# Kernel tuning notes

Hardware: AMD Instinct MI355X
Metric: run time of the kernel (lower is better)

The kernel has to match this reference:

```python
import jax, jax.numpy as jnp
import numpy as np
import math

B, T, D = 2, 2048, 1024
H, DH = 16, 64  # n_heads, d_head
ROPE_THETA = 10000.0


def _rope_cos_sin(seq_len, d_head, dtype):
    # inv_freq over even indices, freqs[i,j] = t_i * inv_freq_j, shape [T, d_head//2]
    inv_freq = 1.0 / (ROPE_THETA ** (jnp.arange(0, d_head, 2, dtype=jnp.float32) / d_head))
    freqs = jnp.arange(seq_len, dtype=jnp.float32)[:, None] * inv_freq[None, :]
    # emb = cat(freqs, freqs); we only ever index cos[..., :d_head//2], so keep the half
    cos = jnp.cos(freqs).astype(dtype)[None, :, None, :]  # [1,T,1,DH/2]
    sin = jnp.sin(freqs).astype(dtype)[None, :, None, :]
    return cos, sin


def _apply_rotation(x, cos, sin):
    # x: [B,T,H,DH]; rotate-half style as in the torch module
    x1, x2 = x[..., : x.shape[-1] // 2], x[..., x.shape[-1] // 2 :]
    return jnp.concatenate([x1 * cos - x2 * sin, x1 * sin + x2 * cos], axis=-1)


def setup_inputs() -> dict:
    key = jax.random.key(0)
    k1, k2, k3 = jax.random.split(key, 3)
    x = jax.random.normal(k1, (B, T, D), dtype=jnp.float32)
    # torch Linear weights stored transposed here as [in, out]; init_std=0.02
    Wqkv = jax.random.normal(k2, (D, 3 * D), dtype=jnp.float32) * 0.02
    Wout = jax.random.normal(k3, (D, D), dtype=jnp.float32) * 0.02
    return {"x": x, "Wqkv": Wqkv, "Wout": Wout}


def reference(x, Wqkv, Wout):
    b, t, d = x.shape
    qkv = x @ Wqkv  # [B,T,3D]
    q, k, v = jnp.split(qkv, 3, axis=-1)
    q = q.reshape(b, t, H, DH)
    k = k.reshape(b, t, H, DH)
    v = v.reshape(b, t, H, DH)

    cos, sin = _rope_cos_sin(t, DH, x.dtype)
    q = _apply_rotation(q, cos, sin)
    k = _apply_rotation(k, cos, sin)

    scale = 1.0 / math.sqrt(DH)
    # scores: [B,H,Tq,Tk]
    scores = jnp.einsum("bqhd,bkhd->bhqk", q, k) * scale
    causal = jnp.triu(jnp.ones((t, t), dtype=bool), k=1)
    scores = jnp.where(causal[None, None, :, :], -jnp.inf, scores)
    attn = jax.nn.softmax(scores, axis=-1)
    # dropout in eval mode -> identity
    out = jnp.einsum("bhqk,bkhd->bqhd", attn, v).reshape(b, t, d)
    return out @ Wout
```

## Files before the change

### kernel.cpp

```cpp
#include <hip/hip_runtime.h>
#include <hip/hip_bf16.h>
#include <stdint.h>
#include <math.h>

#define T_SEQ 2048
#define NHEAD 16
#define NBH   32
#define BTROW 4096

typedef __bf16 bf16_t;
typedef __bf16 bf16x4_t __attribute__((ext_vector_type(4)));
typedef __bf16 bf16x8_t __attribute__((ext_vector_type(8)));
typedef float  f32x4_t  __attribute__((ext_vector_type(4)));

#define QSCALE 0.18033688011112042f

__device__ __forceinline__ f32x4_t mfma16(bf16x8_t a, bf16x8_t b, f32x4_t c) {
  return __builtin_amdgcn_mfma_f32_16x16x32_bf16(a, b, c, 0, 0, 0);
}

__device__ __forceinline__ float fast_exp2(float x) {
#if __has_builtin(__builtin_amdgcn_exp2f)
  return __builtin_amdgcn_exp2f(x);
#else
  return exp2f(x);
#endif
}

__device__ __forceinline__ void gl_lds16(const bf16_t* g, bf16_t* l) {
  __builtin_amdgcn_global_load_lds(
      (const __attribute__((address_space(1))) void*)g,
      (__attribute__((address_space(3))) void*)l, 16, 0, 0);
}

__global__ __launch_bounds__(256) void k_cast_bf16(const float* __restrict__ in,
                                                   bf16_t* __restrict__ out, int n) {
  int tid = blockIdx.x * blockDim.x + threadIdx.x;
  int stride = gridDim.x * blockDim.x;
  for (int i = tid * 4; i < n; i += stride * 4) {
    float4 a = *(const float4*)(in + i);
    bf16x4_t r = { (bf16_t)a.x, (bf16_t)a.y, (bf16_t)a.z, (bf16_t)a.w };
    *(bf16x4_t*)(out + i) = r;
  }
}

__global__ __launch_bounds__(256) void k_trans_cast(const float* __restrict__ W,
                                                    bf16_t* __restrict__ WT,
                                                    int K, int N) {
  __shared__ float tile[32][33];
  int n0 = blockIdx.x * 32, k0 = blockIdx.y * 32;
  int tx = threadIdx.x & 31, ty = threadIdx.x >> 5;
#pragma unroll
  for (int j = 0; j < 4; j++)
    tile[ty + j * 8][tx] = W[(size_t)(k0 + ty + j * 8) * N + n0 + tx];
  __syncthreads();
#pragma unroll
  for (int j = 0; j < 4; j++)
    WT[(size_t)(n0 + ty + j * 8) * K + k0 + tx] = (bf16_t)tile[tx][ty + j * 8];
}

__global__ __launch_bounds__(256) void k_rope_table(float* __restrict__ cs,
                                                    float* __restrict__ sn) {
  int i = blockIdx.x * blockDim.x + threadIdx.x;
  if (i >= T_SEQ * 32) return;
  int t = i >> 5, j = i & 31;
  float inv = powf(10000.0f, -(float)(2 * j) / 64.0f);
  float f = (float)t * inv;
  cs[i] = cosf(f);
  sn[i] = sinf(f);
}

__global__ __launch_bounds__(256) void k_gemm_qkv(const bf16_t* __restrict__ A,
                                                  const bf16_t* __restrict__ Bt,
                                                  const float* __restrict__ cs,
                                                  const float* __restrict__ sn,
                                                  bf16_t* __restrict__ Qr,
                                                  bf16_t* __restrict__ Kr,
                                                  bf16_t* __restrict__ Vt) {
  const int K = 1024;
  __shared__ __align__(16) unsigned char smem[33792];
  bf16_t* vtile = (bf16_t*)smem;

  int m0 = blockIdx.y * 128, n0 = blockIdx.x * 128;
  int tid = threadIdx.x;
  int lane = tid & 63, w = tid >> 6;
  int wr = w >> 1, wc = w & 1;
  int l15 = lane & 15, l4 = lane >> 4;

  f32x4_t acc[4][4];
#pragma unroll
  for (int m = 0; m < 4; m++)
#pragma unroll
    for (int n = 0; n < 4; n++) acc[m][n] = (f32x4_t){0.f, 0.f, 0.f, 0.f};

  auto stageg = [&](int bf, int k0) {
    bf16_t* As = (bf16_t*)(smem + bf * 16384);
    bf16_t* Bs = (bf16_t*)(smem + 8192 + bf * 16384);
#pragma unroll
    for (int j = 0; j < 2; j++) {
      int c = j * 256 + tid;
      int row = c >> 2, kb = c & 3;
      gl_lds16(A + (size_t)(m0 + row) * K + k0 + kb * 8, As + (size_t)(j * 256 + w * 64) * 8);
      gl_lds16(Bt + (size_t)(n0 + row) * K + k0 + kb * 8, Bs + (size_t)(j * 256 + w * 64) * 8);
    }
  };

  stageg(0, 0);
  for (int kt = 0; kt < 32; kt++) {
    int cb = kt & 1;
    bf16_t* As = (bf16_t*)(smem + cb * 16384);
    bf16_t* Bs = (bf16_t*)(smem + 8192 + cb * 16384);
    asm volatile("s_waitcnt vmcnt(0)" ::: "memory");
    __builtin_amdgcn_s_barrier();
    if (kt + 1 < 32) stageg(cb ^ 1, (kt + 1) * 32);
    bf16x8_t af[4], bfr[4];
#pragma unroll
    for (int m = 0; m < 4; m++)
      af[m] = *(const bf16x8_t*)(As + (size_t)(wr * 64 + m * 16 + l15) * 32 + l4 * 8);
#pragma unroll
    for (int n = 0; n < 4; n++)
      bfr[n] = *(const bf16x8_t*)(Bs + (size_t)(wc * 64 + n * 16 + l15) * 32 + l4 * 8);
#pragma unroll
    for (int m = 0; m < 4; m++)
#pragma unroll
      for (int n = 0; n < 4; n++) acc[m][n] = mfma16(af[m], bfr[n], acc[m][n]);
  }
  __syncthreads();

  int region = n0 >> 10;
  if (region < 2) {
    bf16_t* dst = region ? Kr : Qr;
    float qs = region ? 1.0f : QSCALE;
    int h = ((n0 & 1023) + wc * 64) >> 6;
#pragma unroll
    for (int m = 0; m < 4; m++)
#pragma unroll
      for (int r = 0; r < 4; r++) {
        int row = m0 + wr * 64 + m * 16 + l4 * 4 + r;
        int b = row >> 11, t = row & 2047;
        size_t obase = ((size_t)(b * NHEAD + h) * T_SEQ + t) * 64;
#pragma unroll
        for (int n = 0; n < 2; n++) {
          int j = n * 16 + l15;
          float c = cs[t * 32 + j], s = sn[t * 32 + j];
          float x1 = acc[m][n][r], x2 = acc[m][n + 2][r];
          dst[obase + j]      = (bf16_t)((x1 * c - x2 * s) * qs);
          dst[obase + 32 + j] = (bf16_t)((x1 * s + x2 * c) * qs);
        }
      }
  } else {
#pragma unroll
    for (int m = 0; m < 4; m++)
#pragma unroll
      for (int n = 0; n < 4; n++)
#pragma unroll
        for (int r = 0; r < 4; r++)
          vtile[(size_t)(wc * 64 + n * 16 + l15) * 132 + wr * 64 + m * 16 + l4 * 4 + r] =
              (bf16_t)acc[m][n][r];
    __syncthreads();
    int colbase = n0 - 2048;
    int b = m0 >> 11, t0l = m0 & 2047;
#pragma unroll
    for (int p = 0; p < 64; p++) {
      int idx = p * 256 + tid;
      int dl = idx >> 7, tl = idx & 127;
      int col = colbase + dl, h = col >> 6, d = col & 63;
      Vt[((size_t)(b * NHEAD + h) * 64 + d) * T_SEQ + t0l + tl] = vtile[(size_t)dl * 132 + tl];
    }
  }
}

__global__ __launch_bounds__(256) void k_gemm2(const bf16_t* __restrict__ A,
                                               const bf16_t* __restrict__ Bt,
                                               float* __restrict__ C) {
  const int N = 1024, K = 1024;
  __shared__ __align__(16) bf16_t As[2][64 * 32];
  __shared__ __align__(16) bf16_t Bs[2][128 * 32];
  int m0 = blockIdx.y * 64, n0 = blockIdx.x * 128;
  int tid = threadIdx.x;
  int lane = tid & 63, w = tid >> 6;
  int l15 = lane & 15, l4 = lane >> 4;

  f32x4_t acc[4][2];
#pragma unroll
  for (int m = 0; m < 4; m++)
#pragma unroll
    for (int n = 0; n < 2; n++) acc[m][n] = (f32x4_t){0.f, 0.f, 0.f, 0.f};

  auto stageg = [&](int bf, int k0) {
    {
      int row = tid >> 2, kb = tid & 3;
      gl_lds16(A + (size_t)(m0 + row) * K + k0 + kb * 8, &As[bf][0] + (size_t)(w * 64) * 8);
    }
#pragma unroll
    for (int j = 0; j < 2; j++) {
      int c = j * 256 + tid;
      int row = c >> 2, kb = c & 3;
      gl_lds16(Bt + (size_t)(n0 + row) * K + k0 + kb * 8, &Bs[bf][0] + (size_t)(j * 256 + w * 64) * 8);
    }
  };

  stageg(0, 0);
  for (int kt = 0; kt < 32; kt++) {
    int cb = kt & 1;
    asm volatile("s_waitcnt vmcnt(0)" ::: "memory");
    __builtin_amdgcn_s_barrier();
    if (kt + 1 < 32) stageg(cb ^ 1, (kt + 1) * 32);
    bf16x8_t af[4], bfr[2];
#pragma unroll
    for (int m = 0; m < 4; m++)
      af[m] = *(const bf16x8_t*)(&As[cb][0] + (size_t)(m * 16 + l15) * 32 + l4 * 8);
#pragma unroll
    for (int n = 0; n < 2; n++)
      bfr[n] = *(const bf16x8_t*)(&Bs[cb][0] + (size_t)(w * 32 + n * 16 + l15) * 32 + l4 * 8);
#pragma unroll
    for (int m = 0; m < 4; m++)
#pragma unroll
      for (int n = 0; n < 2; n++) acc[m][n] = mfma16(af[m], bfr[n], acc[m][n]);
  }
#pragma unroll
  for (int m = 0; m < 4; m++)
#pragma unroll
    for (int n = 0; n < 2; n++)
#pragma unroll
      for (int r = 0; r < 4; r++) {
        int row = m0 + m * 16 + l4 * 4 + r;
        int col = n0 + w * 32 + n * 16 + l15;
        C[(size_t)row * N + col] = acc[m][n][r];
      }
}

__global__ __launch_bounds__(512, 4) void k_attn(const bf16_t* __restrict__ Qr,
                                                 const bf16_t* __restrict__ Kr,
                                                 const bf16_t* __restrict__ Vt,
                                                 bf16_t* __restrict__ Ob) {
  __shared__ __align__(16) bf16_t Ks[2][2][64 * 64];
  __shared__ __align__(16) bf16_t Vs[2][2][64 * 64];
  __shared__ __align__(16) bf16_t Ps[8][16 * 64];
  int flat = blockIdx.x;
  int swz = (flat & 7) * 64 + (flat >> 3);
  int pair = swz & 15, bh = swz >> 4;
  int b = bh >> 4, h = bh & 15;
  int tid = threadIdx.x, lane = tid & 63, w = tid >> 6;
  int grp = w >> 2, wl = w & 3;
  int l15 = lane & 15, l4 = lane >> 4;

  const bf16_t* Kbh = Kr + (size_t)bh * T_SEQ * 64;
  const bf16_t* Vbh = Vt + (size_t)bh * 64 * T_SEQ;

  int srow = tid >> 3;
  int sk8 = (tid & 7) ^ (srow & 7);

  auto stage = [&](int buf, int i) {
#pragma unroll
    for (int tp = 0; tp < 2; tp++) {
      int kb = (2 * i + tp) * 64;
      gl_lds16(Kbh + (size_t)(kb + srow) * 64 + sk8 * 8, &Ks[buf][tp][0] + (size_t)w * 512);
      gl_lds16(Vbh + (size_t)srow * T_SEQ + kb + sk8 * 8, &Vs[buf][tp][0] + (size_t)w * 512);
    }
  };

  char* myPs = (char*)&Ps[w][0];

  bf16x8_t ones;
#pragma unroll
  for (int i = 0; i < 8; i++) ones[i] = (bf16_t)1.0f;

  for (int pass = 0; pass < 2; pass++) {
    int qb = pass ? (31 - pair) : pair;
    int q0 = qb * 64;
    int niter = (qb + 2) >> 1;

    bf16x8_t qf[2];
    size_t qbase = ((size_t)bh * T_SEQ + q0 + wl * 16 + l15) * 64;
    qf[0] = *(const bf16x8_t*)(Qr + qbase + l4 * 8);
    qf[1] = *(const bf16x8_t*)(Qr + qbase + 32 + l4 * 8);

    f32x4_t o[4];
#pragma unroll
    for (int n = 0; n < 4; n++) o[n] = (f32x4_t){0.f, 0.f, 0.f, 0.f};
    f32x4_t ls = (f32x4_t){0.f, 0.f, 0.f, 0.f};
    float m_s = -1e30f;

    stage(0, 0);

    for (int i = 0; i < niter; i++) {
      int cur = i & 1;
      asm volatile("s_waitcnt vmcnt(0)" ::: "memory");
      __builtin_amdgcn_s_barrier();
      if (i + 1 < niter) stage(cur ^ 1, i + 1);

      int t = 2 * i + grp;
      if (t <= qb) {
        const bf16_t* Kt = &Ks[cur][grp][0];
        const bf16_t* Vtl = &Vs[cur][grp][0];

        f32x4_t s[4];
        __builtin_amdgcn_s_setprio(1);
#pragma unroll
        for (int n = 0; n < 4; n++) {
          int rowK = n * 16 + l15;
          const bf16_t* kp = Kt + (size_t)rowK * 64;
          int sw = rowK & 7;
          bf16x8_t kf0 = *(const bf16x8_t*)(kp + (l4 ^ sw) * 8);
          bf16x8_t kf1 = *(const bf16x8_t*)(kp + ((l4 ^ 4) ^ sw) * 8);
          s[n] = (f32x4_t){0.f, 0.f, 0.f, 0.f};
          s[n] = mfma16(kf0, qf[0], s[n]);
          s[n] = mfma16(kf1, qf[1], s[n]);
        }
        __builtin_amdgcn_s_setprio(0);

        if (t == qb) {
#pragma unroll
          for (int n = 0; n < 4; n++)
#pragma unroll
            for (int r = 0; r < 4; r++)
              if (n * 16 + l4 * 4 + r > wl * 16 + l15) s[n][r] = -1e30f;
        }

        float t0 = fmaxf(fmaxf(s[0][0], s[0][1]), fmaxf(s[0][2], s[0][3]));
        float t1 = fmaxf(fmaxf(s[1][0], s[1][1]), fmaxf(s[1][2], s[1][3]));
        float t2 = fmaxf(fmaxf(s[2][0], s[2][1]), fmaxf(s[2][2], s[2][3]));
        float t3 = fmaxf(fmaxf(s[3][0], s[3][1]), fmaxf(s[3][2], s[3][3]));
        float mx = fmaxf(fmaxf(t0, t1), fmaxf(t2, t3));
        mx = fmaxf(mx, __shfl_xor(mx, 16, 64));
        mx = fmaxf(mx, __shfl_xor(mx, 32, 64));

        if (__any(mx - m_s > 8.0f)) {
          float mnew = fmaxf(m_s, mx);
          float alpha = fast_exp2(m_s - mnew);
          m_s = mnew;
          float ar[4];
#pragma unroll
          for (int r = 0; r < 4; r++) ar[r] = __shfl(alpha, l4 * 4 + r, 64);
#pragma unroll
          for (int n = 0; n < 4; n++)
#pragma unroll
            for (int r = 0; r < 4; r++) o[n][r] *= ar[r];
#pragma unroll
          for (int r = 0; r < 4; r++) ls[r] *= ar[r];
        }

#pragma unroll
        for (int n = 0; n < 4; n++) {
#pragma unroll
          for (int r = 0; r < 4; r++) s[n][r] = fast_exp2(s[n][r] - m_s);
          bf16x4_t pk = { (bf16_t)s[n][0], (bf16_t)s[n][1], (bf16_t)s[n][2], (bf16_t)s[n][3] };
          *(bf16x4_t*)(myPs + l15 * 128 +
                       ((((n << 1) | (l4 >> 1)) ^ (l15 & 7)) << 4) + ((l4 & 1) << 3)) = pk;
        }

        __builtin_amdgcn_s_setprio(1);
#pragma unroll
        for (int ks = 0; ks < 2; ks++) {
          bf16x8_t pa = *(const bf16x8_t*)(myPs + l15 * 128 +
                                           ((((ks << 2) | l4) ^ (l15 & 7)) << 4));
          ls = mfma16(pa, ones, ls);
#pragma unroll
          for (int n = 0; n < 4; n++) {
            int rowV = n * 16 + l15;
            bf16x8_t vf = *(const bf16x8_t*)(Vtl + (size_t)rowV * 64 +
                                             (((ks * 4 + l4) ^ (rowV & 7)) * 8));
            o[n] = mfma16(pa, vf, o[n]);
          }
        }
        __builtin_amdgcn_s_setprio(0);
      }
    }

    __syncthreads();
    float* mg = (float*)&Ks[0][0][0];
    int base = (wl * 64 + lane) * 25;
    if (grp == 1) {
#pragma unroll
      for (int n = 0; n < 4; n++)
#pragma unroll
        for (int r = 0; r < 4; r++) mg[base + n * 4 + r] = o[n][r];
#pragma unroll
      for (int r = 0; r < 4; r++) mg[base + 16 + r] = ls[r];
#pragma unroll
      for (int r = 0; r < 4; r++) mg[base + 20 + r] = __shfl(m_s, l4 * 4 + r, 64);
    }
    __syncthreads();
    if (grp == 0) {
#pragma unroll
      for (int r = 0; r < 4; r++) {
        float mA = __shfl(m_s, l4 * 4 + r, 64);
        float mB = mg[base + 20 + r];
        float mF = fmaxf(mA, mB);
        float fA = fast_exp2(mA - mF), fB = fast_exp2(mB - mF);
        float lF = ls[r] * fA + mg[base + 16 + r] * fB;
        float ir = 1.0f / lF;
        int q = q0 + wl * 16 + l4 * 4 + r;
        size_t off = ((size_t)(b * T_SEQ + q)) * 1024 + h * 64;
#pragma unroll
        for (int n = 0; n < 4; n++) {
          float val = o[n][r] * fA + mg[base + n * 4 + r] * fB;
          Ob[off + n * 16 + l15] = (bf16_t)(val * ir);
        }
      }
    }
    __syncthreads();
  }
}

extern "C" void kernel_launch(void* const* d_in, const int* in_sizes, int n_in,
                              void* d_out, int out_size, void* d_ws, size_t ws_size,
                              hipStream_t stream) {
  const float* x    = (const float*)d_in[0];
  const float* Wqkv = (const float*)d_in[1];
  const float* Wout = (const float*)d_in[2];
  float* out = (float*)d_out;
  char* ws = (char*)d_ws;

  bf16_t* wqkvT = (bf16_t*)(ws + 0);
  bf16_t* woutT = (bf16_t*)(ws + 6291456);
  bf16_t* xb    = (bf16_t*)(ws + 8388608);
  bf16_t* Qr    = (bf16_t*)(ws + 41943040);
  bf16_t* Kr    = (bf16_t*)(ws + 50331648);
  bf16_t* Vt    = (bf16_t*)(ws + 58720256);
  float*  cs    = (float*)(ws + 67108864);
  float*  sn    = (float*)(ws + 67371008);
  bf16_t* Ob    = xb;

  k_cast_bf16<<<2048, 256, 0, stream>>>(x, xb, 4096 * 1024);
  k_trans_cast<<<dim3(3072 / 32, 1024 / 32), 256, 0, stream>>>(Wqkv, wqkvT, 1024, 3072);
  k_trans_cast<<<dim3(1024 / 32, 1024 / 32), 256, 0, stream>>>(Wout, woutT, 1024, 1024);
  k_rope_table<<<(T_SEQ * 32) / 256, 256, 0, stream>>>(cs, sn);

  k_gemm_qkv<<<dim3(3072 / 128, 4096 / 128), 256, 0, stream>>>(xb, wqkvT, cs, sn, Qr, Kr, Vt);
  k_attn<<<512, 512, 0, stream>>>(Qr, Kr, Vt, Ob);
  k_gemm2<<<dim3(1024 / 128, 4096 / 64), 256, 0, stream>>>(Ob, woutT, out);
}
```

Before: 119.1 us.

## Triple-buffer GEMM k-loops and prefetch V fragments early in attention

Both GEMM kernels move from double to triple buffering, prefetching two k-tiles ahead and waiting on a partial vmcnt instead of draining all loads. This is meant to hide global-to-LDS latency, at the cost of more shared memory per block and possibly lower occupancy. In attention, V fragments are loaded into registers right after the QK MFMAs so the LDS reads overlap the softmax. The row-max shuffles now run only when a rescale is triggered, which adds register pressure from the eight held V fragments.

```diff
diff --git a/kernel.cpp b/kernel.cpp
--- a/kernel.cpp
+++ b/kernel.cpp
@@ -77,8 +77,8 @@
                                                   bf16_t* __restrict__ Qr,
                                                   bf16_t* __restrict__ Kr,
                                                   bf16_t* __restrict__ Vt) {
-  const int K = 1024;
-  __shared__ __align__(16) unsigned char smem[33792];
+  const int K = 1024, NT = 32;
+  __shared__ __align__(16) unsigned char smem[49152];
   bf16_t* vtile = (bf16_t*)smem;
 
   int m0 = blockIdx.y * 128, n0 = blockIdx.x * 128;
@@ -106,13 +106,16 @@
   };
 
   stageg(0, 0);
-  for (int kt = 0; kt < 32; kt++) {
-    int cb = kt & 1;
+  stageg(1, 32);
+  for (int kt = 0; kt < NT; kt++) {
+    int cb = kt % 3;
     bf16_t* As = (bf16_t*)(smem + cb * 16384);
     bf16_t* Bs = (bf16_t*)(smem + 8192 + cb * 16384);
-    asm volatile("s_waitcnt vmcnt(0)" ::: "memory");
+    if (kt + 1 < NT) asm volatile("s_waitcnt vmcnt(4)" ::: "memory");
+    else             asm volatile("s_waitcnt vmcnt(0)" ::: "memory");
     __builtin_amdgcn_s_barrier();
-    if (kt + 1 < 32) stageg(cb ^ 1, (kt + 1) * 32);
+    if (kt + 2 < NT) stageg((kt + 2) % 3, (kt + 2) * 32);
+
     bf16x8_t af[4], bfr[4];
 #pragma unroll
     for (int m = 0; m < 4; m++)
@@ -173,9 +176,8 @@
 __global__ __launch_bounds__(256) void k_gemm2(const bf16_t* __restrict__ A,
                                                const bf16_t* __restrict__ Bt,
                                                float* __restrict__ C) {
-  const int N = 1024, K = 1024;
-  __shared__ __align__(16) bf16_t As[2][64 * 32];
-  __shared__ __align__(16) bf16_t Bs[2][128 * 32];
+  const int N = 1024, K = 1024, NT = 32;
+  __shared__ __align__(16) unsigned char smem[36864];
   int m0 = blockIdx.y * 64, n0 = blockIdx.x * 128;
   int tid = threadIdx.x;
   int lane = tid & 63, w = tid >> 6;
@@ -188,31 +190,38 @@
     for (int n = 0; n < 2; n++) acc[m][n] = (f32x4_t){0.f, 0.f, 0.f, 0.f};
 
   auto stageg = [&](int bf, int k0) {
+    bf16_t* As = (bf16_t*)(smem + bf * 12288);
+    bf16_t* Bs = (bf16_t*)(smem + 4096 + bf * 12288);
     {
       int row = tid >> 2, kb = tid & 3;
-      gl_lds16(A + (size_t)(m0 + row) * K + k0 + kb * 8, &As[bf][0] + (size_t)(w * 64) * 8);
+      gl_lds16(A + (size_t)(m0 + row) * K + k0 + kb * 8, As + (size_t)(w * 64) * 8);
     }
 #pragma unroll
     for (int j = 0; j < 2; j++) {
       int c = j * 256 + tid;
       int row = c >> 2, kb = c & 3;
-      gl_lds16(Bt + (size_t)(n0 + row) * K + k0 + kb * 8, &Bs[bf][0] + (size_t)(j * 256 + w * 64) * 8);
+      gl_lds16(Bt + (size_t)(n0 + row) * K + k0 + kb * 8, Bs + (size_t)(j * 256 + w * 64) * 8);
     }
   };
 
   stageg(0, 0);
-  for (int kt = 0; kt < 32; kt++) {
-    int cb = kt & 1;
-    asm volatile("s_waitcnt vmcnt(0)" ::: "memory");
+  stageg(1, 32);
+  for (int kt = 0; kt < NT; kt++) {
+    int cb = kt % 3;
+    bf16_t* As = (bf16_t*)(smem + cb * 12288);
+    bf16_t* Bs = (bf16_t*)(smem + 4096 + cb * 12288);
+    if (kt + 1 < NT) asm volatile("s_waitcnt vmcnt(3)" ::: "memory");
+    else             asm volatile("s_waitcnt vmcnt(0)" ::: "memory");
     __builtin_amdgcn_s_barrier();
-    if (kt + 1 < 32) stageg(cb ^ 1, (kt + 1) * 32);
+    if (kt + 2 < NT) stageg((kt + 2) % 3, (kt + 2) * 32);
+
     bf16x8_t af[4], bfr[2];
 #pragma unroll
     for (int m = 0; m < 4; m++)
-      af[m] = *(const bf16x8_t*)(&As[cb][0] + (size_t)(m * 16 + l15) * 32 + l4 * 8);
+      af[m] = *(const bf16x8_t*)(As + (size_t)(m * 16 + l15) * 32 + l4 * 8);
 #pragma unroll
     for (int n = 0; n < 2; n++)
-      bfr[n] = *(const bf16x8_t*)(&Bs[cb][0] + (size_t)(w * 32 + n * 16 + l15) * 32 + l4 * 8);
+      bfr[n] = *(const bf16x8_t*)(Bs + (size_t)(w * 32 + n * 16 + l15) * 32 + l4 * 8);
 #pragma unroll
     for (int m = 0; m < 4; m++)
 #pragma unroll
@@ -310,6 +319,16 @@
         }
         __builtin_amdgcn_s_setprio(0);
 
+        bf16x8_t vfr[8];
+#pragma unroll
+        for (int ks = 0; ks < 2; ks++)
+#pragma unroll
+          for (int n = 0; n < 4; n++) {
+            int rowV = n * 16 + l15;
+            vfr[ks * 4 + n] = *(const bf16x8_t*)(Vtl + (size_t)rowV * 64 +
+                                                 (((ks * 4 + l4) ^ (rowV & 7)) * 8));
+          }
+
         if (t == qb) {
 #pragma unroll
           for (int n = 0; n < 4; n++)
@@ -322,11 +341,11 @@
         float t1 = fmaxf(fmaxf(s[1][0], s[1][1]), fmaxf(s[1][2], s[1][3]));
         float t2 = fmaxf(fmaxf(s[2][0], s[2][1]), fmaxf(s[2][2], s[2][3]));
         float t3 = fmaxf(fmaxf(s[3][0], s[3][1]), fmaxf(s[3][2], s[3][3]));
-        float mx = fmaxf(fmaxf(t0, t1), fmaxf(t2, t3));
-        mx = fmaxf(mx, __shfl_xor(mx, 16, 64));
-        mx = fmaxf(mx, __shfl_xor(mx, 32, 64));
-
-        if (__any(mx - m_s > 8.0f)) {
+        float mloc = fmaxf(fmaxf(t0, t1), fmaxf(t2, t3));
+
+        if (__any(mloc - m_s > 8.0f)) {
+          float mx = fmaxf(mloc, __shfl_xor(mloc, 16, 64));
+          mx = fmaxf(mx, __shfl_xor(mx, 32, 64));
           float mnew = fmaxf(m_s, mx);
           float alpha = fast_exp2(m_s - mnew);
           m_s = mnew;
@@ -357,12 +376,7 @@
                                            ((((ks << 2) | l4) ^ (l15 & 7)) << 4));
           ls = mfma16(pa, ones, ls);
 #pragma unroll
-          for (int n = 0; n < 4; n++) {
-            int rowV = n * 16 + l15;
-            bf16x8_t vf = *(const bf16x8_t*)(Vtl + (size_t)rowV * 64 +
-                                             (((ks * 4 + l4) ^ (rowV & 7)) * 8));
-            o[n] = mfma16(pa, vf, o[n]);
-          }
+          for (int n = 0; n < 4; n++) o[n] = mfma16(pa, vfr[ks * 4 + n], o[n]);
         }
         __builtin_amdgcn_s_setprio(0);
       }
```

After: 109.1 us. 8.4% less time.
